# Kernel optimization log

Measured on AMD Instinct MI355X. Metric: run time of the kernel, lower is better.

## Reference

```python
import jax, jax.numpy as jnp
import numpy as np

DN = ('NCHW', 'OIHW', 'NCHW')

def _conv(x, W, pad):
    return jax.lax.conv_general_dilated(x, W, (1, 1), [(pad, pad), (pad, pad)], dimension_numbers=DN)

def _cbs(x, W, s, b, pad):
    # Conv2d(bias=False) + folded BatchNorm (scale/bias) + SiLU
    y = _conv(x, W, pad) * s[None, :, None, None] + b[None, :, None, None]
    return y * jax.nn.sigmoid(y)

def _l2norm(x):
    n = jnp.sqrt(jnp.sum(x * x, axis=1, keepdims=True))
    return x / jnp.maximum(n, 1e-12)

def setup_inputs() -> dict:
    key = jax.random.key(0)
    ks = jax.random.split(key, 24)
    B, C, H, L, TD, NC = 16, 256, 64, 40, 768, 8
    EMB = (TD + NC * 2) // 2  # 392
    w = lambda k, sh: jax.random.normal(k, sh, jnp.float32) * 0.02
    img = jax.random.normal(ks[0], (B, C, H, H), jnp.float32)
    flang = jax.random.normal(ks[1], (B, L, TD), jnp.float32)
    lengths = jax.random.randint(ks[2], (B, 1), 5, L + 1)
    word_mask = (jnp.arange(L)[None, :] < lengths).astype(jnp.int32)
    return {
        'img': img, 'flang': flang, 'word_mask': word_mask, 'sigma_w': 0.1,
        'W1': w(ks[3], (EMB, TD)), 'b1': w(ks[4], (EMB,)),
        'W2': w(ks[5], (NC * 2, EMB)), 'b2': w(ks[6], (NC * 2,)),
        'Wv': w(ks[7], (C, C, 1, 1)), 'sv': jnp.ones((C,)), 'bv': w(ks[8], (C,)),
        'Wg': w(ks[9], (NC, NC, 1, 1)), 'sg': jnp.ones((NC,)), 'bg': w(ks[10], (NC,)),
        'Wb': w(ks[11], (NC, NC, 1, 1)), 'sb': jnp.ones((NC,)), 'bb': w(ks[12], (NC,)),
        'Wf1': w(ks[13], (C, C, 1, 1)), 'sf1': jnp.ones((C,)), 'bf1': w(ks[14], (C,)),
        'Wf2': w(ks[15], (C, C, 3, 3)), 'sf2': jnp.ones((C,)), 'bf2': w(ks[16], (C,)),
        'Wf3': w(ks[17], (C, C, 1, 1)), 'bf3': w(ks[18], (C,)),
        'Ws': w(ks[19], (NC, C, 3, 3)), 'bs': w(ks[20], (NC,)),
        'add_weight': jnp.zeros((), jnp.float32),
    }

def reference(img, flang, word_mask, sigma_w, W1, b1, W2, b2, Wv, sv, bv,
              Wg, sg, bg, Wb, sb, bb, Wf1, sf1, bf1, Wf2, sf2, bf2,
              Wf3, bf3, Ws, bs, add_weight):
    B, C, H = img.shape[0], img.shape[1], img.shape[2]
    nc = Wg.shape[0]
    map_visu = jnp.tanh(_cbs(img, Wv, sv, bv, 0))
    # ragged masked mean excluding first (CLS) and last (SEP) masked tokens
    m = word_mask.astype(jnp.float32)
    c = jnp.cumsum(m, axis=1)
    tot = c[:, -1:]
    inc = m * ((c > 1) & (c < tot)).astype(jnp.float32)  # [B,L]
    flang_avg = jnp.sum(flang * inc[:, :, None], axis=1) / jnp.sum(inc, axis=1, keepdims=True)
    map_flang = jax.nn.sigmoid((flang_avg @ W1.T + b1) @ W2.T + b2)  # [B,2*nc]
    maps = map_flang.reshape(B, nc, 2)
    sigma_x = sigma_w * H
    sig = _conv(img, Ws, 0) + bs[None, :, None, None]  # [B,nc,H-2,H-2]
    sigma_weight = jax.nn.sigmoid(jnp.mean(sig, axis=(2, 3), keepdims=True))  # [B,nc,1,1]
    sigma_y = sigma_x * sigma_weight
    yc = (maps[:, :, 0] * H).astype(jnp.int32).astype(jnp.float32)[:, :, None, None]
    xc = (maps[:, :, 1] * H).astype(jnp.int32).astype(jnp.float32)[:, :, None, None]
    gy = jnp.arange(H, dtype=jnp.float32)[None, None, :, None]
    gx = jnp.arange(H, dtype=jnp.float32)[None, None, None, :]
    weights = jnp.exp(-((gy - yc) ** 2 / (2.0 * sigma_y ** 2) + (gx - xc) ** 2 / (2.0 * sigma_x ** 2)))  # [B,nc,H,H]
    gamma = jnp.tanh(_cbs(weights, Wg, sg, bg, 0))
    beta = jnp.tanh(_cbs(weights, Wb, sb, bb, 0))
    g = jnp.mean(gamma, axis=1, keepdims=True)
    bmax = jnp.max(beta, axis=1, keepdims=True)
    v_film = _l2norm(g * map_visu + bmax)
    v_film = _cbs(v_film, Wf1, sf1, bf1, 0)
    v_film = _cbs(v_film, Wf2, sf2, bf2, 1)
    v_film = _conv(v_film, Wf3, 0) + bf3[None, :, None, None]
    aw = jnp.tanh(add_weight)
    v_add = (1.0 + aw) * img + (1.0 - aw) * v_film
    return _l2norm(v_add)
```

## Files before the change

### kernel.cpp

```cpp
#include <hip/hip_runtime.h>
#include <hip/hip_bf16.h>


#define DEVFN static __device__ __forceinline__

DEVFN float sigmoidf_(float x) { return 1.f / (1.f + expf(-x)); }
DEVFN float siluf_(float y) { return y / (1.f + __expf(-y)); }
DEVFN float tanh_fast_(float x) { return 1.f - 2.f / (__expf(2.f * x) + 1.f); }

typedef __attribute__((ext_vector_type(8))) short bf16x8;
typedef __attribute__((ext_vector_type(4))) float f32x4;

DEVFN unsigned short f2bf_(float f) {
    union { __hip_bfloat16 b; unsigned short u; } cv;
    cv.b = __float2bfloat16(f);
    return cv.u;
}
DEVFN float bf2f_(unsigned short u) {
    union { unsigned short u; __hip_bfloat16 b; } cv;
    cv.u = u;
    return __bfloat162float(cv.b);
}

DEVFN void async_cp16(const void* g, void* l) {
    __builtin_amdgcn_global_load_lds(
        (const __attribute__((address_space(1))) unsigned int*)g,
        (__attribute__((address_space(3))) unsigned int*)l, 16, 0, 0);
}

__global__ void prep_kernel(const float* __restrict__ Wv, const float* __restrict__ Wf1,
                            const float* __restrict__ Wf3, const float* __restrict__ Wf2,
                            short* __restrict__ WvB, short* __restrict__ W1B,
                            short* __restrict__ W3B, short* __restrict__ WB2,
                            float* __restrict__ zbuf) {
    int idx = blockIdx.x * 256 + threadIdx.x;
    if (idx < 8) zbuf[idx] = 0.f;
    if (idx < 65536) {
        int j    = idx & 7;
        int lane = (idx >> 3) & 63;
        int coT  = (idx >> 9) & 15;
        int ci32 = (idx >> 13) & 7;
        int co = coT * 16 + (lane & 15);
        int ci = ci32 * 32 + ((lane >> 4) << 3) + j;
        int src = co * 256 + ci;
        WvB[idx] = (short)f2bf_(Wv[src]);
        W1B[idx] = (short)f2bf_(Wf1[src]);
        W3B[idx] = (short)f2bf_(Wf3[src]);
    }
    int o = idx - 65536;
    if (o >= 0 && o < 589824) {
        int j    = o & 7;
        int lane = (o >> 3) & 63;
        int coT  = (o >> 9) & 15;
        int ci32 = (o >> 13) & 7;
        int kk   = o >> 16;
        int co = coT * 16 + (lane & 15);
        int ci = ci32 * 32 + ((lane >> 4) << 3) + j;
        WB2[o] = (short)f2bf_(Wf2[(co * 256 + ci) * 9 + kk]);
    }
}

__global__ void langmlp_kernel(const float* __restrict__ flang, const int* __restrict__ mask,
                               const float* __restrict__ W1, const float* __restrict__ b1,
                               const float* __restrict__ W2, const float* __restrict__ b2,
                               float* __restrict__ ycxc) {
    __shared__ float inc[40];
    __shared__ float isum;
    __shared__ float fa[768];
    __shared__ float h[392];
    __shared__ float o[16];
    int b = blockIdx.x, t = threadIdx.x;
    if (t == 0) {
        float cum[40];
        float c = 0.f;
        for (int l = 0; l < 40; ++l) { c += (float)mask[b * 40 + l]; cum[l] = c; }
        float tot = c, s = 0.f;
        for (int l = 0; l < 40; ++l) {
            float m = (float)mask[b * 40 + l];
            float v = (cum[l] > 1.f && cum[l] < tot) ? m : 0.f;
            inc[l] = v; s += v;
        }
        isum = s;
    }
    __syncthreads();
    for (int d = t; d < 768; d += 448) {
        float a = 0.f;
        for (int l = 0; l < 40; ++l) a += flang[(size_t)(b * 40 + l) * 768 + d] * inc[l];
        fa[d] = a / isum;
    }
    __syncthreads();
    if (t < 392) {
        float a = b1[t];
        const float* w = W1 + (size_t)t * 768;
        for (int k = 0; k < 768; ++k) a = fmaf(fa[k], w[k], a);
        h[t] = a;
    }
    __syncthreads();
    if (t < 16) {
        float a = b2[t];
        const float* w = W2 + (size_t)t * 392;
        for (int k = 0; k < 392; ++k) a = fmaf(h[k], w[k], a);
        o[t] = sigmoidf_(a);
    }
    __syncthreads();
    if (t < 8) {
        ycxc[b * 8 + t]       = (float)(int)(o[2 * t] * 64.f);
        ycxc[128 + b * 8 + t] = (float)(int)(o[2 * t + 1] * 64.f);
    }
}

__global__ void wsum_kernel(const float* __restrict__ img, float* __restrict__ S) {
    __shared__ float red[9 * 256];
    int bc = blockIdx.x;
    int t = threadIdx.x;
    float s[9];
#pragma unroll
    for (int k = 0; k < 9; ++k) s[k] = 0.f;
    const float* p = img + (size_t)bc * 4096;
    for (int j = 0; j < 16; ++j) {
        int idx = t + j * 256;
        int y = idx >> 6, x = idx & 63;
        float v = p[idx];
#pragma unroll
        for (int ky = 0; ky < 3; ++ky) {
            if (y < ky || y > ky + 61) continue;
#pragma unroll
            for (int kx = 0; kx < 3; ++kx) {
                if (x < kx || x > kx + 61) continue;
                s[ky * 3 + kx] += v;
            }
        }
    }
#pragma unroll
    for (int k = 0; k < 9; ++k) red[k * 256 + t] = s[k];
    __syncthreads();
    for (int st = 128; st > 0; st >>= 1) {
        if (t < st) {
#pragma unroll
            for (int k = 0; k < 9; ++k) red[k * 256 + t] += red[k * 256 + t + st];
        }
        __syncthreads();
    }
    if (t < 9) S[(size_t)bc * 9 + t] = red[t * 256];
}

__global__ void sigw_kernel(const float* __restrict__ Ws, const float* __restrict__ S,
                            const float* __restrict__ bs, float* __restrict__ sigw) {
    __shared__ float red[8 * 256];
    int b = blockIdx.x, t = threadIdx.x;
    float sv[9];
    const float* Sp = S + (size_t)(b * 256 + t) * 9;
#pragma unroll
    for (int k = 0; k < 9; ++k) sv[k] = Sp[k];
#pragma unroll
    for (int co = 0; co < 8; ++co) {
        const float* wp = Ws + (size_t)(co * 256 + t) * 9;
        float a = 0.f;
#pragma unroll
        for (int k = 0; k < 9; ++k) a = fmaf(wp[k], sv[k], a);
        red[co * 256 + t] = a;
    }
    __syncthreads();
    for (int st = 128; st > 0; st >>= 1) {
        if (t < st) {
#pragma unroll
            for (int co = 0; co < 8; ++co) red[co * 256 + t] += red[co * 256 + t + st];
        }
        __syncthreads();
    }
    if (t < 8) sigw[b * 8 + t] = sigmoidf_(red[t * 256] / 3844.f + bs[t]);
}

__global__ void gauss_kernel(const float* __restrict__ ycxc, const float* __restrict__ sigw,
                             const float* __restrict__ sigma_w,
                             const float* __restrict__ Wg, const float* __restrict__ sg,
                             const float* __restrict__ bg,
                             const float* __restrict__ Wb, const float* __restrict__ sb,
                             const float* __restrict__ bb,
                             float* __restrict__ g, float* __restrict__ bm) {
    int blk = blockIdx.x;
    int b = blk >> 6, y = blk & 63;
    int x = threadIdx.x;
    float sx = sigma_w[0] * 64.f;
    float w[8];
#pragma unroll
    for (int n = 0; n < 8; ++n) {
        float yc = ycxc[b * 8 + n], xc = ycxc[128 + b * 8 + n];
        float sy = sx * sigw[b * 8 + n];
        float dy = (float)y - yc, dx = (float)x - xc;
        w[n] = expf(-(dy * dy / (2.f * sy * sy) + dx * dx / (2.f * sx * sx)));
    }
    float gacc = 0.f, bmax = -3.4e38f;
#pragma unroll
    for (int n = 0; n < 8; ++n) {
        float a1 = 0.f, a2 = 0.f;
#pragma unroll
        for (int m = 0; m < 8; ++m) {
            a1 = fmaf(Wg[n * 8 + m], w[m], a1);
            a2 = fmaf(Wb[n * 8 + m], w[m], a2);
        }
        float ga = tanhf(siluf_(a1 * sg[n] + bg[n]));
        float be = tanhf(siluf_(a2 * sb[n] + bb[n]));
        gacc += ga;
        bmax = fmaxf(bmax, be);
    }
    g[(size_t)(b * 64 + y) * 64 + x] = gacc * 0.125f;
    bm[(size_t)(b * 64 + y) * 64 + x] = bmax;
}

__global__ __launch_bounds__(256) void f01_kernel(
        const float* __restrict__ img, const short* __restrict__ wvb,
        const short* __restrict__ w1b,
        const float* __restrict__ sv, const float* __restrict__ bv,
        const float* __restrict__ s1, const float* __restrict__ b1,
        const float* __restrict__ g, const float* __restrict__ bm,
        __hip_bfloat16* __restrict__ outB) {
    __shared__ __attribute__((aligned(16))) short lA[64 * 264];
    __shared__ float invs[64];
    __shared__ float ls_sv[256], ls_bv[256], ls_s1[256], ls_b1[256];
    __shared__ float ls_g[64], ls_bm[64];
    float* pr = (float*)lA;
    int blk = blockIdx.x, b = blk >> 6, y = blk & 63;
    int t = threadIdx.x, w = t >> 6, lane = t & 63;
    int lx = lane & 15, koct = lane >> 4;

    ls_sv[t] = sv[t]; ls_bv[t] = bv[t];
    ls_s1[t] = s1[t]; ls_b1[t] = b1[t];
    if (t < 64) {
        ls_g[t]  = g[(size_t)(b * 64 + y) * 64 + t];
        ls_bm[t] = bm[(size_t)(b * 64 + y) * 64 + t];
    }

    {
        int x = t & 63, cg = t >> 6;
        const float* ib = img + (size_t)b * 1048576 + y * 64 + x;
#pragma unroll
        for (int c8 = 0; c8 < 8; ++c8) {
            int ci0 = cg * 64 + c8 * 8;
            unsigned short r[8];
#pragma unroll
            for (int j = 0; j < 8; ++j) r[j] = f2bf_(ib[(size_t)(ci0 + j) * 4096]);
            *(uint4*)&lA[x * 264 + ci0] = *(uint4*)r;
        }
    }
    f32x4 acc[4][4];
#pragma unroll
    for (int mi = 0; mi < 4; ++mi)
#pragma unroll
        for (int ni = 0; ni < 4; ++ni) acc[mi][ni] = (f32x4){0.f, 0.f, 0.f, 0.f};
    __syncthreads();

#pragma unroll
    for (int k32 = 0; k32 < 8; ++k32) {
        const short* wp = wvb + (((k32 * 16) + w * 4) * 64 + lane) * 8;
        bf16x8 bfr[4];
#pragma unroll
        for (int ni = 0; ni < 4; ++ni) bfr[ni] = *(const bf16x8*)(wp + ni * 512);
        bf16x8 afr[4];
#pragma unroll
        for (int mi = 0; mi < 4; ++mi)
            afr[mi] = *(const bf16x8*)&lA[(mi * 16 + lx) * 264 + k32 * 32 + koct * 8];
#pragma unroll
        for (int mi = 0; mi < 4; ++mi)
#pragma unroll
            for (int ni = 0; ni < 4; ++ni)
                acc[mi][ni] = __builtin_amdgcn_mfma_f32_16x16x32_bf16(afr[mi], bfr[ni], acc[mi][ni], 0, 0, 0);
    }
    __syncthreads();

#pragma unroll
    for (int mi = 0; mi < 4; ++mi)
#pragma unroll
        for (int rr = 0; rr < 4; ++rr) {
            int x = mi * 16 + koct * 4 + rr;
            float ps = 0.f;
#pragma unroll
            for (int ni = 0; ni < 4; ++ni) {
                int co = w * 64 + ni * 16 + lx;
                float yv = fmaf(acc[mi][ni][rr], ls_sv[co], ls_bv[co]);
                float mvv = tanh_fast_(siluf_(yv));
                float v = fmaf(ls_g[x], mvv, ls_bm[x]);
                acc[mi][ni][rr] = v;
                ps += v * v;
            }
            pr[x * 64 + w * 16 + lx] = ps;
        }
    __syncthreads();
    if (t < 64) {
        float s2 = 0.f;
        for (int q = 0; q < 64; ++q) s2 += pr[t * 64 + q];
        invs[t] = 1.f / fmaxf(sqrtf(s2), 1e-12f);
    }
    __syncthreads();

#pragma unroll
    for (int mi = 0; mi < 4; ++mi)
#pragma unroll
        for (int ni = 0; ni < 4; ++ni) {
            int co = w * 64 + ni * 16 + lx;
#pragma unroll
            for (int rr = 0; rr < 4; ++rr) {
                int x = mi * 16 + koct * 4 + rr;
                lA[x * 264 + co] = (short)f2bf_(acc[mi][ni][rr] * invs[x]);
            }
        }
#pragma unroll
    for (int mi = 0; mi < 4; ++mi)
#pragma unroll
        for (int ni = 0; ni < 4; ++ni) acc[mi][ni] = (f32x4){0.f, 0.f, 0.f, 0.f};
    __syncthreads();

#pragma unroll
    for (int k32 = 0; k32 < 8; ++k32) {
        const short* wp = w1b + (((k32 * 16) + w * 4) * 64 + lane) * 8;
        bf16x8 bfr[4];
#pragma unroll
        for (int ni = 0; ni < 4; ++ni) bfr[ni] = *(const bf16x8*)(wp + ni * 512);
        bf16x8 afr[4];
#pragma unroll
        for (int mi = 0; mi < 4; ++mi)
            afr[mi] = *(const bf16x8*)&lA[(mi * 16 + lx) * 264 + k32 * 32 + koct * 8];
#pragma unroll
        for (int mi = 0; mi < 4; ++mi)
#pragma unroll
            for (int ni = 0; ni < 4; ++ni)
                acc[mi][ni] = __builtin_amdgcn_mfma_f32_16x16x32_bf16(afr[mi], bfr[ni], acc[mi][ni], 0, 0, 0);
    }
    __syncthreads();

#pragma unroll
    for (int mi = 0; mi < 4; ++mi)
#pragma unroll
        for (int ni = 0; ni < 4; ++ni) {
            int co = w * 64 + ni * 16 + lx;
#pragma unroll
            for (int rr = 0; rr < 4; ++rr) {
                int x = mi * 16 + koct * 4 + rr;
                float yv = fmaf(acc[mi][ni][rr], ls_s1[co], ls_b1[co]);
                lA[x * 264 + co] = (short)f2bf_(siluf_(yv));
            }
        }
    __syncthreads();
    unsigned short* og = (unsigned short*)outB + (size_t)(b * 64 + y) * 16384;
#pragma unroll
    for (int it = 0; it < 8; ++it) {
        int e8 = t + it * 256;
        int x2 = e8 >> 5, c8 = e8 & 31;
        *(uint4*)(og + e8 * 8) = *(uint4*)&lA[x2 * 264 + c8 * 8];
    }
}

DEVFN void stage_chunk(const unsigned short* __restrict__ xg, short* ldsbuf,
                       const unsigned short* __restrict__ zbuf, int cc, int y0, int t) {
#pragma unroll
    for (int p = 0; p < 10; ++p) {
        int slot = t + p * 256;
        if (slot < 2376) {
            int r = slot / 594;
            int rem = slot - r * 594;
            int xp = rem / 9;
            int oct = rem - xp * 9;
            int ys = y0 + r - 1, xs = xp - 1;
            bool valid = (oct < 8) && (ys >= 0) && (ys < 64) && (xs >= 0) && (xs < 64);
            const unsigned short* gp = valid ? (xg + ((ys * 64 + xs) * 256 + cc * 64 + oct * 8))
                                             : zbuf;
            async_cp16(gp, ldsbuf + slot * 8);
        }
    }
}

__global__ __launch_bounds__(256, 2) void conv3x3_mfma(const __hip_bfloat16* __restrict__ xin,
                                                       const short* __restrict__ wb,
                                                       const float* __restrict__ sc,
                                                       const float* __restrict__ bi,
                                                       const float* __restrict__ zbufF,
                                                       __hip_bfloat16* __restrict__ outB) {
    __shared__ __attribute__((aligned(16))) short lds[2][19008];
    int blk = blockIdx.x;
    int b = blk >> 5, y0 = (blk & 31) * 2;
    int t = threadIdx.x;
    int w = t >> 6, lane = t & 63;
    int lx = lane & 15, koct = lane >> 4;
    const unsigned short* xg = (const unsigned short*)xin + (size_t)b * 1048576;
    const unsigned short* zbuf = (const unsigned short*)zbufF;

    f32x4 acc[8][4];
#pragma unroll
    for (int mi = 0; mi < 8; ++mi)
#pragma unroll
        for (int ni = 0; ni < 4; ++ni) acc[mi][ni] = (f32x4){0.f, 0.f, 0.f, 0.f};

    stage_chunk(xg, lds[0], zbuf, 0, y0, t);
    __syncthreads();

    for (int cc = 0; cc < 4; ++cc) {
        short* cur = lds[cc & 1];
        if (cc < 3) stage_chunk(xg, lds[(cc + 1) & 1], zbuf, cc + 1, y0, t);
        for (int kk = 0; kk < 9; ++kk) {
            int ky = kk / 3, kx = kk - ky * 3;
#pragma unroll
            for (int k32 = 0; k32 < 2; ++k32) {
                const short* wp = wb + ((((kk * 8 + cc * 2 + k32) * 16) + w * 4) * 64 + lane) * 8;
                bf16x8 bfr[4];
#pragma unroll
                for (int ni = 0; ni < 4; ++ni)
                    bfr[ni] = *(const bf16x8*)(wp + ni * 512);
                bf16x8 afr[8];
#pragma unroll
                for (int mi = 0; mi < 8; ++mi) {
                    int row = mi >> 2, xb = (mi & 3) * 16;
                    afr[mi] = *(const bf16x8*)&cur[((row + ky) * 66 + xb + lx + kx) * 72 + k32 * 32 + koct * 8];
                }
#pragma unroll
                for (int mi = 0; mi < 8; ++mi)
#pragma unroll
                    for (int ni = 0; ni < 4; ++ni)
                        acc[mi][ni] = __builtin_amdgcn_mfma_f32_16x16x32_bf16(afr[mi], bfr[ni], acc[mi][ni], 0, 0, 0);
            }
        }
        __syncthreads();
    }
    short* ep = &lds[0][0];
#pragma unroll
    for (int r2 = 0; r2 < 2; ++r2) {
#pragma unroll
        for (int mi4 = 0; mi4 < 4; ++mi4) {
            int mi = r2 * 4 + mi4;
#pragma unroll
            for (int ni = 0; ni < 4; ++ni) {
                int co = w * 64 + ni * 16 + lx;
                float s = sc[co], bb2 = bi[co];
#pragma unroll
                for (int rr = 0; rr < 4; ++rr) {
                    int x = mi4 * 16 + koct * 4 + rr;
                    float yv = fmaf(acc[mi][ni][rr], s, bb2);
                    ep[x * 264 + co] = (short)f2bf_(siluf_(yv));
                }
            }
        }
        __syncthreads();
        unsigned short* og = (unsigned short*)outB + (size_t)(b * 64 + y0 + r2) * 16384;
#pragma unroll
        for (int it = 0; it < 8; ++it) {
            int e8 = t + it * 256;
            int x2 = e8 >> 5, c8 = e8 & 31;
            *(uint4*)(og + e8 * 8) = *(uint4*)&ep[x2 * 264 + c8 * 8];
        }
        __syncthreads();
    }
}

__global__ __launch_bounds__(256, 4) void final_mfma(const __hip_bfloat16* __restrict__ inB,
                                                     const short* __restrict__ w3b,
                                                     const float* __restrict__ bf3,
                                                     const float* __restrict__ img,
                                                     const float* __restrict__ addw,
                                                     float* __restrict__ outF) {
    __shared__ __attribute__((aligned(16))) short lA[64 * 264];
    __shared__ float pr2[256];
    __shared__ float invs[64];
    __shared__ float ls_b[256];
    int blk = blockIdx.x, b = blk >> 6, y = blk & 63;
    int t = threadIdx.x, w = t >> 6, lane = t & 63;
    int lx = lane & 15, koct = lane >> 4;
    ls_b[t] = bf3[t];

    const unsigned short* xg = (const unsigned short*)inB + (size_t)(b * 64 + y) * 16384;
#pragma unroll
    for (int it = 0; it < 8; ++it) {
        int e8 = t + it * 256;
        int x2 = e8 >> 5, c8 = e8 & 31;
        *(uint4*)&lA[x2 * 264 + c8 * 8] = *(const uint4*)(xg + e8 * 8);
    }
    f32x4 acc[4][4];
#pragma unroll
    for (int mi = 0; mi < 4; ++mi)
#pragma unroll
        for (int ni = 0; ni < 4; ++ni) acc[mi][ni] = (f32x4){0.f, 0.f, 0.f, 0.f};
    __syncthreads();

#pragma unroll
    for (int k32 = 0; k32 < 8; ++k32) {
        const short* wp = w3b + (((k32 * 16) + w * 4) * 64 + lane) * 8;
        bf16x8 bfr[4];
#pragma unroll
        for (int ni = 0; ni < 4; ++ni) bfr[ni] = *(const bf16x8*)(wp + ni * 512);
        bf16x8 afr[4];
#pragma unroll
        for (int mi = 0; mi < 4; ++mi)
            afr[mi] = *(const bf16x8*)&lA[(mi * 16 + lx) * 264 + k32 * 32 + koct * 8];
#pragma unroll
        for (int mi = 0; mi < 4; ++mi)
#pragma unroll
            for (int ni = 0; ni < 4; ++ni)
                acc[mi][ni] = __builtin_amdgcn_mfma_f32_16x16x32_bf16(afr[mi], bfr[ni], acc[mi][ni], 0, 0, 0);
    }
    __syncthreads();

#pragma unroll
    for (int mi = 0; mi < 4; ++mi)
#pragma unroll
        for (int ni = 0; ni < 4; ++ni) {
            int co = w * 64 + ni * 16 + lx;
            float b3 = ls_b[co];
#pragma unroll
            for (int rr = 0; rr < 4; ++rr) {
                int x = mi * 16 + koct * 4 + rr;
                lA[co * 66 + x] = (short)f2bf_(acc[mi][ni][rr] + b3);
            }
        }
    __syncthreads();

    float aw = tanhf(addw[0]);
    float ca = 1.f + aw, cb = 1.f - aw;
    int x = t & 63, cg = t >> 6;
    const float* ip = img + (size_t)b * 1048576 + y * 64 + x;
    float ss = 0.f;
#pragma unroll 8
    for (int j = 0; j < 64; ++j) {
        int co = cg * 64 + j;
        float v = fmaf(cb, bf2f_((unsigned short)lA[co * 66 + x]), ca * ip[(size_t)co * 4096]);
        ss += v * v;
    }
    pr2[cg * 64 + x] = ss;
    __syncthreads();
    if (t < 64)
        invs[t] = 1.f / fmaxf(sqrtf(pr2[t] + pr2[64 + t] + pr2[128 + t] + pr2[192 + t]), 1e-12f);
    __syncthreads();
    float iv = invs[x];
    float* op = outF + (size_t)b * 1048576 + y * 64 + x;
#pragma unroll 8
    for (int j = 0; j < 64; ++j) {
        int co = cg * 64 + j;
        float v = fmaf(cb, bf2f_((unsigned short)lA[co * 66 + x]), ca * ip[(size_t)co * 4096]);
        op[(size_t)co * 4096] = v * iv;
    }
}

extern "C" void kernel_launch(void* const* d_in, const int* in_sizes, int n_in,
                              void* d_out, int out_size, void* d_ws, size_t ws_size,
                              hipStream_t stream) {
    const float* img     = (const float*)d_in[0];
    const float* flang   = (const float*)d_in[1];
    const int*   wmask   = (const int*)d_in[2];
    const float* sigma_w = (const float*)d_in[3];
    const float* W1      = (const float*)d_in[4];
    const float* b1      = (const float*)d_in[5];
    const float* W2      = (const float*)d_in[6];
    const float* b2      = (const float*)d_in[7];
    const float* Wv      = (const float*)d_in[8];
    const float* sv      = (const float*)d_in[9];
    const float* bv      = (const float*)d_in[10];
    const float* Wg      = (const float*)d_in[11];
    const float* sg      = (const float*)d_in[12];
    const float* bg      = (const float*)d_in[13];
    const float* Wb      = (const float*)d_in[14];
    const float* sb      = (const float*)d_in[15];
    const float* bb      = (const float*)d_in[16];
    const float* Wf1     = (const float*)d_in[17];
    const float* sf1     = (const float*)d_in[18];
    const float* bf1     = (const float*)d_in[19];
    const float* Wf2     = (const float*)d_in[20];
    const float* sf2     = (const float*)d_in[21];
    const float* bf2     = (const float*)d_in[22];
    const float* Wf3     = (const float*)d_in[23];
    const float* bf3     = (const float*)d_in[24];
    const float* Ws      = (const float*)d_in[25];
    const float* bs      = (const float*)d_in[26];
    const float* addw    = (const float*)d_in[27];
    float* out = (float*)d_out;
    float* ws  = (float*)d_ws;

    short* WvB  = (short*)ws;
    short* W1B  = (short*)(ws + 32768);
    short* W3B  = (short*)(ws + 65536);
    short* WB2  = (short*)(ws + 98304);
    float* ycxc = ws + 405504;
    float* S    = ws + 405760;
    float* sigw = ws + 442624;
    float* gmap = ws + 442752;
    float* bmap = ws + 508288;
    float* zbuf = ws + 573824;
    __hip_bfloat16* bufA = (__hip_bfloat16*)(ws + 573840);
    __hip_bfloat16* bufB = (__hip_bfloat16*)(ws + 8962448);

    prep_kernel<<<2560, 256, 0, stream>>>(Wv, Wf1, Wf3, Wf2, WvB, W1B, W3B, WB2, zbuf);
    langmlp_kernel<<<16, 448, 0, stream>>>(flang, wmask, W1, b1, W2, b2, ycxc);
    wsum_kernel<<<4096, 256, 0, stream>>>(img, S);
    sigw_kernel<<<16, 256, 0, stream>>>(Ws, S, bs, sigw);
    gauss_kernel<<<1024, 64, 0, stream>>>(ycxc, sigw, sigma_w, Wg, sg, bg, Wb, sb, bb, gmap, bmap);
    f01_kernel<<<1024, 256, 0, stream>>>(img, WvB, W1B, sv, bv, sf1, bf1, gmap, bmap, bufB);
    conv3x3_mfma<<<512, 256, 0, stream>>>(bufB, WB2, sf2, bf2, zbuf, bufA);
    final_mfma<<<1024, 256, 0, stream>>>(bufA, W3B, bf3, img, addw, out);
}
```

Measured before the change: 419.5 us.

## Fuse pipeline into three kernels: mega prep, f01 with gauss, conv3x3 with final

```diff
diff --git a/kernel.cpp b/kernel.cpp
--- a/kernel.cpp
+++ b/kernel.cpp
@@ -28,184 +28,122 @@
         (__attribute__((address_space(3))) unsigned int*)l, 16, 0, 0);
 }
 
-__global__ void prep_kernel(const float* __restrict__ Wv, const float* __restrict__ Wf1,
-                            const float* __restrict__ Wf3, const float* __restrict__ Wf2,
-                            short* __restrict__ WvB, short* __restrict__ W1B,
-                            short* __restrict__ W3B, short* __restrict__ WB2,
-                            float* __restrict__ zbuf) {
-    int idx = blockIdx.x * 256 + threadIdx.x;
-    if (idx < 8) zbuf[idx] = 0.f;
-    if (idx < 65536) {
-        int j    = idx & 7;
-        int lane = (idx >> 3) & 63;
-        int coT  = (idx >> 9) & 15;
-        int ci32 = (idx >> 13) & 7;
-        int co = coT * 16 + (lane & 15);
-        int ci = ci32 * 32 + ((lane >> 4) << 3) + j;
-        int src = co * 256 + ci;
-        WvB[idx] = (short)f2bf_(Wv[src]);
-        W1B[idx] = (short)f2bf_(Wf1[src]);
-        W3B[idx] = (short)f2bf_(Wf3[src]);
-    }
-    int o = idx - 65536;
-    if (o >= 0 && o < 589824) {
-        int j    = o & 7;
-        int lane = (o >> 3) & 63;
-        int coT  = (o >> 9) & 15;
-        int ci32 = (o >> 13) & 7;
-        int kk   = o >> 16;
-        int co = coT * 16 + (lane & 15);
-        int ci = ci32 * 32 + ((lane >> 4) << 3) + j;
-        WB2[o] = (short)f2bf_(Wf2[(co * 256 + ci) * 9 + kk]);
-    }
-}
-
-__global__ void langmlp_kernel(const float* __restrict__ flang, const int* __restrict__ mask,
-                               const float* __restrict__ W1, const float* __restrict__ b1,
-                               const float* __restrict__ W2, const float* __restrict__ b2,
-                               float* __restrict__ ycxc) {
+__global__ __launch_bounds__(256) void mega1_kernel(
+        const float* __restrict__ Wv, const float* __restrict__ Wf1,
+        const float* __restrict__ Wf3, const float* __restrict__ Wf2,
+        short* __restrict__ WvB, short* __restrict__ W1B,
+        short* __restrict__ W3B, short* __restrict__ WB2,
+        float* __restrict__ zbuf,
+        const float* __restrict__ img, float* __restrict__ S,
+        const float* __restrict__ flang, const int* __restrict__ mask,
+        const float* __restrict__ Wm1, const float* __restrict__ bm1,
+        const float* __restrict__ Wm2, const float* __restrict__ bm2,
+        float* __restrict__ ycxc) {
+    __shared__ float red[9 * 256];
     __shared__ float inc[40];
     __shared__ float isum;
     __shared__ float fa[768];
     __shared__ float h[392];
     __shared__ float o[16];
-    int b = blockIdx.x, t = threadIdx.x;
-    if (t == 0) {
-        float cum[40];
-        float c = 0.f;
-        for (int l = 0; l < 40; ++l) { c += (float)mask[b * 40 + l]; cum[l] = c; }
-        float tot = c, s = 0.f;
-        for (int l = 0; l < 40; ++l) {
-            float m = (float)mask[b * 40 + l];
-            float v = (cum[l] > 1.f && cum[l] < tot) ? m : 0.f;
-            inc[l] = v; s += v;
-        }
-        isum = s;
-    }
-    __syncthreads();
-    for (int d = t; d < 768; d += 448) {
-        float a = 0.f;
-        for (int l = 0; l < 40; ++l) a += flang[(size_t)(b * 40 + l) * 768 + d] * inc[l];
-        fa[d] = a / isum;
-    }
-    __syncthreads();
-    if (t < 392) {
-        float a = b1[t];
-        const float* w = W1 + (size_t)t * 768;
-        for (int k = 0; k < 768; ++k) a = fmaf(fa[k], w[k], a);
-        h[t] = a;
-    }
-    __syncthreads();
-    if (t < 16) {
-        float a = b2[t];
-        const float* w = W2 + (size_t)t * 392;
-        for (int k = 0; k < 392; ++k) a = fmaf(h[k], w[k], a);
-        o[t] = sigmoidf_(a);
-    }
-    __syncthreads();
-    if (t < 8) {
-        ycxc[b * 8 + t]       = (float)(int)(o[2 * t] * 64.f);
-        ycxc[128 + b * 8 + t] = (float)(int)(o[2 * t + 1] * 64.f);
-    }
-}
-
-__global__ void wsum_kernel(const float* __restrict__ img, float* __restrict__ S) {
-    __shared__ float red[9 * 256];
-    int bc = blockIdx.x;
-    int t = threadIdx.x;
-    float s[9];
-#pragma unroll
-    for (int k = 0; k < 9; ++k) s[k] = 0.f;
-    const float* p = img + (size_t)bc * 4096;
-    for (int j = 0; j < 16; ++j) {
-        int idx = t + j * 256;
-        int y = idx >> 6, x = idx & 63;
-        float v = p[idx];
-#pragma unroll
-        for (int ky = 0; ky < 3; ++ky) {
-            if (y < ky || y > ky + 61) continue;
-#pragma unroll
-            for (int kx = 0; kx < 3; ++kx) {
-                if (x < kx || x > kx + 61) continue;
-                s[ky * 3 + kx] += v;
-            }
-        }
-    }
-#pragma unroll
-    for (int k = 0; k < 9; ++k) red[k * 256 + t] = s[k];
-    __syncthreads();
-    for (int st = 128; st > 0; st >>= 1) {
-        if (t < st) {
-#pragma unroll
-            for (int k = 0; k < 9; ++k) red[k * 256 + t] += red[k * 256 + t + st];
-        }
-        __syncthreads();
-    }
-    if (t < 9) S[(size_t)bc * 9 + t] = red[t * 256];
-}
-
-__global__ void sigw_kernel(const float* __restrict__ Ws, const float* __restrict__ S,
-                            const float* __restrict__ bs, float* __restrict__ sigw) {
-    __shared__ float red[8 * 256];
-    int b = blockIdx.x, t = threadIdx.x;
-    float sv[9];
-    const float* Sp = S + (size_t)(b * 256 + t) * 9;
-#pragma unroll
-    for (int k = 0; k < 9; ++k) sv[k] = Sp[k];
-#pragma unroll
-    for (int co = 0; co < 8; ++co) {
-        const float* wp = Ws + (size_t)(co * 256 + t) * 9;
-        float a = 0.f;
-#pragma unroll
-        for (int k = 0; k < 9; ++k) a = fmaf(wp[k], sv[k], a);
-        red[co * 256 + t] = a;
-    }
-    __syncthreads();
-    for (int st = 128; st > 0; st >>= 1) {
-        if (t < st) {
-#pragma unroll
-            for (int co = 0; co < 8; ++co) red[co * 256 + t] += red[co * 256 + t + st];
-        }
-        __syncthreads();
-    }
-    if (t < 8) sigw[b * 8 + t] = sigmoidf_(red[t * 256] / 3844.f + bs[t]);
-}
-
-__global__ void gauss_kernel(const float* __restrict__ ycxc, const float* __restrict__ sigw,
-                             const float* __restrict__ sigma_w,
-                             const float* __restrict__ Wg, const float* __restrict__ sg,
-                             const float* __restrict__ bg,
-                             const float* __restrict__ Wb, const float* __restrict__ sb,
-                             const float* __restrict__ bb,
-                             float* __restrict__ g, float* __restrict__ bm) {
-    int blk = blockIdx.x;
-    int b = blk >> 6, y = blk & 63;
-    int x = threadIdx.x;
-    float sx = sigma_w[0] * 64.f;
-    float w[8];
-#pragma unroll
-    for (int n = 0; n < 8; ++n) {
-        float yc = ycxc[b * 8 + n], xc = ycxc[128 + b * 8 + n];
-        float sy = sx * sigw[b * 8 + n];
-        float dy = (float)y - yc, dx = (float)x - xc;
-        w[n] = expf(-(dy * dy / (2.f * sy * sy) + dx * dx / (2.f * sx * sx)));
-    }
-    float gacc = 0.f, bmax = -3.4e38f;
-#pragma unroll
-    for (int n = 0; n < 8; ++n) {
-        float a1 = 0.f, a2 = 0.f;
-#pragma unroll
-        for (int m = 0; m < 8; ++m) {
-            a1 = fmaf(Wg[n * 8 + m], w[m], a1);
-            a2 = fmaf(Wb[n * 8 + m], w[m], a2);
-        }
-        float ga = tanhf(siluf_(a1 * sg[n] + bg[n]));
-        float be = tanhf(siluf_(a2 * sb[n] + bb[n]));
-        gacc += ga;
-        bmax = fmaxf(bmax, be);
-    }
-    g[(size_t)(b * 64 + y) * 64 + x] = gacc * 0.125f;
-    bm[(size_t)(b * 64 + y) * 64 + x] = bmax;
+    int bid = blockIdx.x, t = threadIdx.x;
+
+    if (bid < 2560) {
+        int idx = bid * 256 + t;
+        if (idx < 8) zbuf[idx] = 0.f;
+        if (idx < 65536) {
+            int j    = idx & 7;
+            int lane = (idx >> 3) & 63;
+            int coT  = (idx >> 9) & 15;
+            int ci32 = (idx >> 13) & 7;
+            int co = coT * 16 + (lane & 15);
+            int ci = ci32 * 32 + ((lane >> 4) << 3) + j;
+            int src = co * 256 + ci;
+            WvB[idx] = (short)f2bf_(Wv[src]);
+            W1B[idx] = (short)f2bf_(Wf1[src]);
+            W3B[idx] = (short)f2bf_(Wf3[src]);
+        }
+        int oo = idx - 65536;
+        if (oo >= 0 && oo < 589824) {
+            int j    = oo & 7;
+            int lane = (oo >> 3) & 63;
+            int coT  = (oo >> 9) & 15;
+            int ci32 = (oo >> 13) & 7;
+            int kk   = oo >> 16;
+            int co = coT * 16 + (lane & 15);
+            int ci = ci32 * 32 + ((lane >> 4) << 3) + j;
+            WB2[oo] = (short)f2bf_(Wf2[(co * 256 + ci) * 9 + kk]);
+        }
+    } else if (bid < 6656) {
+        int bc = bid - 2560;
+        float s[9];
+#pragma unroll
+        for (int k = 0; k < 9; ++k) s[k] = 0.f;
+        const float* p = img + (size_t)bc * 4096;
+        for (int j = 0; j < 16; ++j) {
+            int idx = t + j * 256;
+            int y = idx >> 6, x = idx & 63;
+            float v = p[idx];
+#pragma unroll
+            for (int ky = 0; ky < 3; ++ky) {
+                if (y < ky || y > ky + 61) continue;
+#pragma unroll
+                for (int kx = 0; kx < 3; ++kx) {
+                    if (x < kx || x > kx + 61) continue;
+                    s[ky * 3 + kx] += v;
+                }
+            }
+        }
+#pragma unroll
+        for (int k = 0; k < 9; ++k) red[k * 256 + t] = s[k];
+        __syncthreads();
+        for (int st = 128; st > 0; st >>= 1) {
+            if (t < st) {
+#pragma unroll
+                for (int k = 0; k < 9; ++k) red[k * 256 + t] += red[k * 256 + t + st];
+            }
+            __syncthreads();
+        }
+        if (t < 9) S[(size_t)bc * 9 + t] = red[t * 256];
+    } else {
+        int b = bid - 6656;
+        if (t == 0) {
+            float cum[40];
+            float c = 0.f;
+            for (int l = 0; l < 40; ++l) { c += (float)mask[b * 40 + l]; cum[l] = c; }
+            float tot = c, sm = 0.f;
+            for (int l = 0; l < 40; ++l) {
+                float m = (float)mask[b * 40 + l];
+                float v = (cum[l] > 1.f && cum[l] < tot) ? m : 0.f;
+                inc[l] = v; sm += v;
+            }
+            isum = sm;
+        }
+        __syncthreads();
+        for (int d = t; d < 768; d += 256) {
+            float a = 0.f;
+            for (int l = 0; l < 40; ++l) a += flang[(size_t)(b * 40 + l) * 768 + d] * inc[l];
+            fa[d] = a / isum;
+        }
+        __syncthreads();
+        for (int u = t; u < 392; u += 256) {
+            float a = bm1[u];
+            const float* w = Wm1 + (size_t)u * 768;
+            for (int k = 0; k < 768; ++k) a = fmaf(fa[k], w[k], a);
+            h[u] = a;
+        }
+        __syncthreads();
+        if (t < 16) {
+            float a = bm2[t];
+            const float* w = Wm2 + (size_t)t * 392;
+            for (int k = 0; k < 392; ++k) a = fmaf(h[k], w[k], a);
+            o[t] = sigmoidf_(a);
+        }
+        __syncthreads();
+        if (t < 8) {
+            ycxc[b * 8 + t]       = (float)(int)(o[2 * t] * 64.f);
+            ycxc[128 + b * 8 + t] = (float)(int)(o[2 * t + 1] * 64.f);
+        }
+    }
 }
 
 __global__ __launch_bounds__(256) void f01_kernel(
@@ -213,22 +151,79 @@
         const short* __restrict__ w1b,
         const float* __restrict__ sv, const float* __restrict__ bv,
         const float* __restrict__ s1, const float* __restrict__ b1,
-        const float* __restrict__ g, const float* __restrict__ bm,
+        const float* __restrict__ S, const float* __restrict__ Ws,
+        const float* __restrict__ bs, const float* __restrict__ ycxc,
+        const float* __restrict__ sigma_w,
+        const float* __restrict__ Wg, const float* __restrict__ sg,
+        const float* __restrict__ bg,
+        const float* __restrict__ Wb, const float* __restrict__ sb,
+        const float* __restrict__ bb,
         __hip_bfloat16* __restrict__ outB) {
     __shared__ __attribute__((aligned(16))) short lA[64 * 264];
     __shared__ float invs[64];
     __shared__ float ls_sv[256], ls_bv[256], ls_s1[256], ls_b1[256];
     __shared__ float ls_g[64], ls_bm[64];
-    float* pr = (float*)lA;
+    __shared__ float sigw8[8];
+    float* red = (float*)lA;
+    float* pr  = (float*)lA;
     int blk = blockIdx.x, b = blk >> 6, y = blk & 63;
     int t = threadIdx.x, w = t >> 6, lane = t & 63;
     int lx = lane & 15, koct = lane >> 4;
 
     ls_sv[t] = sv[t]; ls_bv[t] = bv[t];
     ls_s1[t] = s1[t]; ls_b1[t] = b1[t];
+
+    {
+        float s9[9];
+        const float* Sp = S + (size_t)(b * 256 + t) * 9;
+#pragma unroll
+        for (int k = 0; k < 9; ++k) s9[k] = Sp[k];
+#pragma unroll
+        for (int co = 0; co < 8; ++co) {
+            const float* wp = Ws + (size_t)(co * 256 + t) * 9;
+            float a = 0.f;
+#pragma unroll
+            for (int k = 0; k < 9; ++k) a = fmaf(wp[k], s9[k], a);
+            red[co * 256 + t] = a;
+        }
+        __syncthreads();
+        for (int st = 128; st > 0; st >>= 1) {
+            if (t < st) {
+#pragma unroll
+                for (int co = 0; co < 8; ++co) red[co * 256 + t] += red[co * 256 + t + st];
+            }
+            __syncthreads();
+        }
+        if (t < 8) sigw8[t] = sigmoidf_(red[t * 256] / 3844.f + bs[t]);
+        __syncthreads();
+    }
+
     if (t < 64) {
-        ls_g[t]  = g[(size_t)(b * 64 + y) * 64 + t];
-        ls_bm[t] = bm[(size_t)(b * 64 + y) * 64 + t];
+        float sx = sigma_w[0] * 64.f;
+        float wv8[8];
+#pragma unroll
+        for (int n = 0; n < 8; ++n) {
+            float yc = ycxc[b * 8 + n], xc = ycxc[128 + b * 8 + n];
+            float sy = sx * sigw8[n];
+            float dy = (float)y - yc, dx = (float)t - xc;
+            wv8[n] = expf(-(dy * dy / (2.f * sy * sy) + dx * dx / (2.f * sx * sx)));
+        }
+        float gacc = 0.f, bmax = -3.4e38f;
+#pragma unroll
+        for (int n = 0; n < 8; ++n) {
+            float a1 = 0.f, a2 = 0.f;
+#pragma unroll
+            for (int m = 0; m < 8; ++m) {
+                a1 = fmaf(Wg[n * 8 + m], wv8[m], a1);
+                a2 = fmaf(Wb[n * 8 + m], wv8[m], a2);
+            }
+            float ga = tanhf(siluf_(a1 * sg[n] + bg[n]));
+            float be = tanhf(siluf_(a2 * sb[n] + bb[n]));
+            gacc += ga;
+            bmax = fmaxf(bmax, be);
+        }
+        ls_g[t]  = gacc * 0.125f;
+        ls_bm[t] = bmax;
     }
 
     {
@@ -369,13 +364,20 @@
     }
 }
 
-__global__ __launch_bounds__(256, 2) void conv3x3_mfma(const __hip_bfloat16* __restrict__ xin,
-                                                       const short* __restrict__ wb,
-                                                       const float* __restrict__ sc,
-                                                       const float* __restrict__ bi,
-                                                       const float* __restrict__ zbufF,
-                                                       __hip_bfloat16* __restrict__ outB) {
+__global__ __launch_bounds__(256, 2) void c3f_kernel(const __hip_bfloat16* __restrict__ xin,
+                                                     const short* __restrict__ wb,
+                                                     const float* __restrict__ sc,
+                                                     const float* __restrict__ bi,
+                                                     const float* __restrict__ zbufF,
+                                                     const short* __restrict__ w3b,
+                                                     const float* __restrict__ bf3,
+                                                     const float* __restrict__ img,
+                                                     const float* __restrict__ addw,
+                                                     float* __restrict__ outF) {
     __shared__ __attribute__((aligned(16))) short lds[2][19008];
+    __shared__ float pr2[256];
+    __shared__ float invs[64];
+    __shared__ float ls_b3[256];
     int blk = blockIdx.x;
     int b = blk >> 5, y0 = (blk & 31) * 2;
     int t = threadIdx.x;
@@ -383,6 +385,7 @@
     int lx = lane & 15, koct = lane >> 4;
     const unsigned short* xg = (const unsigned short*)xin + (size_t)b * 1048576;
     const unsigned short* zbuf = (const unsigned short*)zbufF;
+    ls_b3[t] = bf3[t];
 
     f32x4 acc[8][4];
 #pragma unroll
@@ -420,7 +423,11 @@
         }
         __syncthreads();
     }
-    short* ep = &lds[0][0];
+
+    float aw = tanhf(addw[0]);
+    float ca = 1.f + aw, cb = 1.f - aw;
+    short* ep  = &lds[0][0];
+    short* wst = &lds[1][0];
 #pragma unroll
     for (int r2 = 0; r2 < 2; ++r2) {
 #pragma unroll
@@ -439,101 +446,63 @@
             }
         }
         __syncthreads();
-        unsigned short* og = (unsigned short*)outB + (size_t)(b * 64 + y0 + r2) * 16384;
-#pragma unroll
-        for (int it = 0; it < 8; ++it) {
-            int e8 = t + it * 256;
-            int x2 = e8 >> 5, c8 = e8 & 31;
-            *(uint4*)(og + e8 * 8) = *(uint4*)&ep[x2 * 264 + c8 * 8];
-        }
-        __syncthreads();
-    }
-}
-
-__global__ __launch_bounds__(256, 4) void final_mfma(const __hip_bfloat16* __restrict__ inB,
-                                                     const short* __restrict__ w3b,
-                                                     const float* __restrict__ bf3,
-                                                     const float* __restrict__ img,
-                                                     const float* __restrict__ addw,
-                                                     float* __restrict__ outF) {
-    __shared__ __attribute__((aligned(16))) short lA[64 * 264];
-    __shared__ float pr2[256];
-    __shared__ float invs[64];
-    __shared__ float ls_b[256];
-    int blk = blockIdx.x, b = blk >> 6, y = blk & 63;
-    int t = threadIdx.x, w = t >> 6, lane = t & 63;
-    int lx = lane & 15, koct = lane >> 4;
-    ls_b[t] = bf3[t];
-
-    const unsigned short* xg = (const unsigned short*)inB + (size_t)(b * 64 + y) * 16384;
-#pragma unroll
-    for (int it = 0; it < 8; ++it) {
-        int e8 = t + it * 256;
-        int x2 = e8 >> 5, c8 = e8 & 31;
-        *(uint4*)&lA[x2 * 264 + c8 * 8] = *(const uint4*)(xg + e8 * 8);
-    }
-    f32x4 acc[4][4];
-#pragma unroll
-    for (int mi = 0; mi < 4; ++mi)
-#pragma unroll
-        for (int ni = 0; ni < 4; ++ni) acc[mi][ni] = (f32x4){0.f, 0.f, 0.f, 0.f};
-    __syncthreads();
-
-#pragma unroll
-    for (int k32 = 0; k32 < 8; ++k32) {
-        const short* wp = w3b + (((k32 * 16) + w * 4) * 64 + lane) * 8;
-        bf16x8 bfr[4];
-#pragma unroll
-        for (int ni = 0; ni < 4; ++ni) bfr[ni] = *(const bf16x8*)(wp + ni * 512);
-        bf16x8 afr[4];
+        f32x4 acc2[4][4];
 #pragma unroll
         for (int mi = 0; mi < 4; ++mi)
-            afr[mi] = *(const bf16x8*)&lA[(mi * 16 + lx) * 264 + k32 * 32 + koct * 8];
+#pragma unroll
+            for (int ni = 0; ni < 4; ++ni) acc2[mi][ni] = (f32x4){0.f, 0.f, 0.f, 0.f};
+#pragma unroll
+        for (int k32 = 0; k32 < 8; ++k32) {
+            const short* wp = w3b + (((k32 * 16) + w * 4) * 64 + lane) * 8;
+            bf16x8 bfr[4];
+#pragma unroll
+            for (int ni = 0; ni < 4; ++ni) bfr[ni] = *(const bf16x8*)(wp + ni * 512);
+            bf16x8 afr[4];
+#pragma unroll
+            for (int mi = 0; mi < 4; ++mi)
+                afr[mi] = *(const bf16x8*)&ep[(mi * 16 + lx) * 264 + k32 * 32 + koct * 8];
+#pragma unroll
+            for (int mi = 0; mi < 4; ++mi)
+#pragma unroll
+                for (int ni = 0; ni < 4; ++ni)
+                    acc2[mi][ni] = __builtin_amdgcn_mfma_f32_16x16x32_bf16(afr[mi], bfr[ni], acc2[mi][ni], 0, 0, 0);
+        }
 #pragma unroll
         for (int mi = 0; mi < 4; ++mi)
 #pragma unroll
-            for (int ni = 0; ni < 4; ++ni)
-                acc[mi][ni] = __builtin_amdgcn_mfma_f32_16x16x32_bf16(afr[mi], bfr[ni], acc[mi][ni], 0, 0, 0);
-    }
-    __syncthreads();
-
-#pragma unroll
-    for (int mi = 0; mi < 4; ++mi)
-#pragma unroll
-        for (int ni = 0; ni < 4; ++ni) {
-            int co = w * 64 + ni * 16 + lx;
-            float b3 = ls_b[co];
-#pragma unroll
-            for (int rr = 0; rr < 4; ++rr) {
-                int x = mi * 16 + koct * 4 + rr;
-                lA[co * 66 + x] = (short)f2bf_(acc[mi][ni][rr] + b3);
-            }
-        }
-    __syncthreads();
-
-    float aw = tanhf(addw[0]);
-    float ca = 1.f + aw, cb = 1.f - aw;
-    int x = t & 63, cg = t >> 6;
-    const float* ip = img + (size_t)b * 1048576 + y * 64 + x;
-    float ss = 0.f;
+            for (int ni = 0; ni < 4; ++ni) {
+                int co = w * 64 + ni * 16 + lx;
+                float b3 = ls_b3[co];
+#pragma unroll
+                for (int rr = 0; rr < 4; ++rr) {
+                    int x = mi * 16 + koct * 4 + rr;
+                    wst[co * 66 + x] = (short)f2bf_(acc2[mi][ni][rr] + b3);
+                }
+            }
+        __syncthreads();
+        int x = t & 63, cg = t >> 6;
+        const float* ip = img + (size_t)b * 1048576 + (size_t)(y0 + r2) * 64 + x;
+        float ss = 0.f;
 #pragma unroll 8
-    for (int j = 0; j < 64; ++j) {
-        int co = cg * 64 + j;
-        float v = fmaf(cb, bf2f_((unsigned short)lA[co * 66 + x]), ca * ip[(size_t)co * 4096]);
-        ss += v * v;
-    }
-    pr2[cg * 64 + x] = ss;
-    __syncthreads();
-    if (t < 64)
-        invs[t] = 1.f / fmaxf(sqrtf(pr2[t] + pr2[64 + t] + pr2[128 + t] + pr2[192 + t]), 1e-12f);
-    __syncthreads();
-    float iv = invs[x];
-    float* op = outF + (size_t)b * 1048576 + y * 64 + x;
+        for (int j = 0; j < 64; ++j) {
+            int co = cg * 64 + j;
+            float v = fmaf(cb, bf2f_((unsigned short)wst[co * 66 + x]), ca * ip[(size_t)co * 4096]);
+            ss += v * v;
+        }
+        pr2[cg * 64 + x] = ss;
+        __syncthreads();
+        if (t < 64)
+            invs[t] = 1.f / fmaxf(sqrtf(pr2[t] + pr2[64 + t] + pr2[128 + t] + pr2[192 + t]), 1e-12f);
+        __syncthreads();
+        float iv = invs[x];
+        float* op = outF + (size_t)b * 1048576 + (size_t)(y0 + r2) * 64 + x;
 #pragma unroll 8
-    for (int j = 0; j < 64; ++j) {
-        int co = cg * 64 + j;
-        float v = fmaf(cb, bf2f_((unsigned short)lA[co * 66 + x]), ca * ip[(size_t)co * 4096]);
-        op[(size_t)co * 4096] = v * iv;
+        for (int j = 0; j < 64; ++j) {
+            int co = cg * 64 + j;
+            float v = fmaf(cb, bf2f_((unsigned short)wst[co * 66 + x]), ca * ip[(size_t)co * 4096]);
+            op[(size_t)co * 4096] = v * iv;
+        }
+        __syncthreads();
     }
 }
 
@@ -575,21 +544,15 @@
     short* W1B  = (short*)(ws + 32768);
     short* W3B  = (short*)(ws + 65536);
     short* WB2  = (short*)(ws + 98304);
-    float* ycxc = ws + 405504;
-    float* S    = ws + 405760;
-    float* sigw = ws + 442624;
-    float* gmap = ws + 442752;
-    float* bmap = ws + 508288;
-    float* zbuf = ws + 573824;
-    __hip_bfloat16* bufA = (__hip_bfloat16*)(ws + 573840);
-    __hip_bfloat16* bufB = (__hip_bfloat16*)(ws + 8962448);
-
-    prep_kernel<<<2560, 256, 0, stream>>>(Wv, Wf1, Wf3, Wf2, WvB, W1B, W3B, WB2, zbuf);
-    langmlp_kernel<<<16, 448, 0, stream>>>(flang, wmask, W1, b1, W2, b2, ycxc);
-    wsum_kernel<<<4096, 256, 0, stream>>>(img, S);
-    sigw_kernel<<<16, 256, 0, stream>>>(Ws, S, bs, sigw);
-    gauss_kernel<<<1024, 64, 0, stream>>>(ycxc, sigw, sigma_w, Wg, sg, bg, Wb, sb, bb, gmap, bmap);
-    f01_kernel<<<1024, 256, 0, stream>>>(img, WvB, W1B, sv, bv, sf1, bf1, gmap, bmap, bufB);
-    conv3x3_mfma<<<512, 256, 0, stream>>>(bufB, WB2, sf2, bf2, zbuf, bufA);
-    final_mfma<<<1024, 256, 0, stream>>>(bufA, W3B, bf3, img, addw, out);
-}
+    float* ycxc = ws + 393216;
+    float* S    = ws + 393472;
+    float* zbuf = ws + 430336;
+    __hip_bfloat16* bufB = (__hip_bfloat16*)(ws + 430352);
+
+    mega1_kernel<<<6672, 256, 0, stream>>>(Wv, Wf1, Wf3, Wf2, WvB, W1B, W3B, WB2, zbuf,
+                                           img, S, flang, wmask, W1, b1, W2, b2, ycxc);
+    f01_kernel<<<1024, 256, 0, stream>>>(img, WvB, W1B, sv, bv, sf1, bf1,
+                                         S, Ws, bs, ycxc, sigma_w,
+                                         Wg, sg, bg, Wb, sb, bb, bufB);
+    c3f_kernel<<<512, 256, 0, stream>>>(bufB, WB2, sf2, bf2, zbuf, W3B, bf3, img, addw, out);
+}
```

Measured after the change: 416.0 us. No clear change (-0.8%).
